# Kernel tuning notes

Measured on AMD Instinct MI355X. Metric: run time of the kernel, lower is better.

The kernel has to match this reference:

```python
import jax, jax.numpy as jnp
import numpy as np

N_LAYERS = 4
EPS = 1e-5  # eqx.nn.LayerNorm default


def _kernels(lam, P, B, C, step, L):
    # Annotated-S4 DPLR generating-function kernel (Q = P), vectorized over H channels.
    # lam, P, B, C: (H, N) complex64; step: (H, 1) real. Returns K: (H, L) real.
    omega = jnp.exp((-2j * jnp.pi) * (jnp.arange(L) / L))            # (L,) roots of unity
    g = (2.0 / step) * ((1.0 - omega) / (1.0 + omega))[None, :]      # (H, L) bilinear warp
    c = 2.0 / (1.0 + omega)                                          # (L,)

    def cauchy(v):  # v: (H, N) -> (H, L): sum_n v_n / (g - lambda_n)
        return jnp.sum(v[:, None, :] / (g[:, :, None] - lam[:, None, :]), axis=-1)

    k00 = cauchy(jnp.conj(C) * B)
    k01 = cauchy(jnp.conj(C) * P)
    k10 = cauchy(jnp.conj(P) * B)
    k11 = cauchy(jnp.conj(P) * P)
    at_roots = c[None, :] * (k00 - k01 * (1.0 / (1.0 + k11)) * k10)  # woodbury correction
    return jnp.fft.ifft(at_roots, n=L, axis=-1).real                 # (H, L)


def _causal_conv(u, K):
    # u: (B, L, H) real input, K: (H, L) real kernel -> causal conv along L via zero-padded FFT.
    L = u.shape[1]
    Ud = jnp.fft.rfft(u, n=2 * L, axis=1)                 # (B, F, H)
    Kd = jnp.fft.rfft(K, n=2 * L, axis=-1)                # (H, F)
    return jnp.fft.irfft(Ud * Kd.T[None], n=2 * L, axis=1)[:, :L]


def _forward(x, enc_w, enc_b, dec_w, dec_b, lam_re, lam_im, p_re, p_im, b_re, b_im,
             c_re, c_im, d, log_step, norm_w, norm_b, w1, b1, w2, b2):
    L = x.shape[1]
    h = x @ enc_w.T + enc_b                               # encoder: (B, L, H)
    for i in range(N_LAYERS):
        skip = h
        mu = h.mean(-1, keepdims=True)
        var = ((h - mu) ** 2).mean(-1, keepdims=True)
        hn = (h - mu) / jnp.sqrt(var + EPS) * norm_w[i] + norm_b[i]
        K = _kernels(lam_re[i] + 1j * lam_im[i], p_re[i] + 1j * p_im[i],
                     b_re[i] + 1j * b_im[i], c_re[i] + 1j * c_im[i],
                     jnp.exp(log_step[i])[:, None], L)
        y = _causal_conv(hn, K) + hn * d[i]               # SSM conv + skip-through D term
        y = jax.nn.gelu(y)
        y = (y @ w1[i].T + b1[i]) * jax.nn.sigmoid(y @ w2[i].T + b2[i])  # gated MLP
        h = skip + y
    return h @ dec_w.T + dec_b                            # decoder: (B, L, out)


def setup_inputs() -> dict:
    key = jax.random.key(0)
    B, L, IN, OUT, H, N, NL = 8, 2048, 64, 64, 128, 64, N_LAYERS
    ks = jax.random.split(key, 12)
    rn = lambda k, s, sc: (jax.random.normal(k, s) * sc).astype(jnp.float32)
    return dict(
        x=rn(ks[0], (B, L, IN), 1.0),
        convolve=1,
        enc_w=rn(ks[1], (H, IN), 1.0 / np.sqrt(IN)), enc_b=jnp.zeros((H,), jnp.float32),
        dec_w=rn(ks[2], (OUT, H), 1.0 / np.sqrt(H)), dec_b=jnp.zeros((OUT,), jnp.float32),
        lam_re=-0.5 * jnp.ones((NL, H, N), jnp.float32),  # HiPPO/S4D-style stable poles
        lam_im=jnp.tile(jnp.float32(np.pi) * jnp.arange(N, dtype=jnp.float32), (NL, H, 1)),
        p_re=rn(ks[3], (NL, H, N), 0.5 / np.sqrt(N)), p_im=rn(ks[4], (NL, H, N), 0.5 / np.sqrt(N)),
        b_re=rn(ks[5], (NL, H, N), 1.0), b_im=rn(ks[6], (NL, H, N), 1.0),
        c_re=rn(ks[7], (NL, H, N), 1.0 / np.sqrt(N)), c_im=rn(ks[8], (NL, H, N), 1.0 / np.sqrt(N)),
        d=jnp.ones((NL, H), jnp.float32),
        log_step=(jax.random.uniform(ks[9], (NL, H)) * (np.log(0.1) - np.log(0.001))
                  + np.log(0.001)).astype(jnp.float32),
        norm_w=jnp.ones((NL, H), jnp.float32), norm_b=jnp.zeros((NL, H), jnp.float32),
        w1=rn(ks[10], (NL, H, H), 1.0 / np.sqrt(H)), b1=jnp.zeros((NL, H), jnp.float32),
        w2=rn(ks[11], (NL, H, H), 1.0 / np.sqrt(H)), b2=jnp.zeros((NL, H), jnp.float32),
    )


def reference(x, convolve, enc_w, enc_b, dec_w, dec_b, lam_re, lam_im, p_re, p_im,
              b_re, b_im, c_re, c_im, d, log_step, norm_w, norm_b, w1, b1, w2, b2):
    # convolve is static 1 (True): the FFT-convolution path of the S4 Model.
    return _forward(x, enc_w, enc_b, dec_w, dec_b, lam_re, lam_im, p_re, p_im, b_re, b_im,
                    c_re, c_im, d, log_step, norm_w, norm_b, w1, b1, w2, b2)
```

## Files before the change

kernel.cpp:

```cpp
#include <hip/hip_runtime.h>
#include <hip/hip_bf16.h>


#define Bsz 8
#define Lseq 2048
#define Hdim 128
#define Npol 64
#define NLAYERS 4

typedef __bf16 bf16x8 __attribute__((ext_vector_type(8)));
typedef float f32x16 __attribute__((ext_vector_type(16)));

__device__ __forceinline__ float fast_rcp(float x) { return __builtin_amdgcn_rcpf(x); }
__device__ __forceinline__ float fast_rsq(float x) { return __builtin_amdgcn_rsqf(x); }

__device__ __forceinline__ float2 cmulf(float2 a, float2 b) {
    return make_float2(a.x * b.x - a.y * b.y, a.x * b.y + a.y * b.x);
}
__device__ __forceinline__ float2 cmulc(float2 a, float2 b) {
    return make_float2(a.x * b.x + a.y * b.y, a.y * b.x - a.x * b.y);
}

__device__ __forceinline__ float gelu_f(float v) {
    float z = 0.7978845608028654f * (v + 0.044715f * v * v * v);
    float e = __expf(2.0f * z);
    return v - v * fast_rcp(e + 1.0f);
}

__device__ __forceinline__ int sw(int i) { return (i & ~15) | ((i ^ (i >> 4)) & 15); }

static __device__ const float W16R[8] = {1.f, 0.9238795325f, 0.7071067812f, 0.3826834324f,
                                         0.f, -0.3826834324f, -0.7071067812f, -0.9238795325f};
static __device__ const float W16I[8] = {0.f, -0.3826834324f, -0.7071067812f, -0.9238795325f,
                                         -1.f, -0.9238795325f, -0.7071067812f, -0.3826834324f};
static __device__ const int BR4[16] = {0, 8, 4, 12, 2, 10, 6, 14, 1, 9, 5, 13, 3, 11, 7, 15};
static __device__ const int BR3[8] = {0, 4, 2, 6, 1, 5, 3, 7};

__device__ __forceinline__ float2 twget(const float2* __restrict__ tw, int e) {
    float2 w = tw[e & 2047];
    if (e & 2048) { w.x = -w.x; w.y = -w.y; }
    return w;
}

template <bool INV>
__device__ __forceinline__ void fft16_dif(float2 v[16]) {
#pragma unroll
    for (int mi = 0; mi < 4; mi++) {
        const int m = 8 >> mi;
#pragma unroll
        for (int g = 0; g < 16; g += 2 * m) {
#pragma unroll
            for (int j = 0; j < m; j++) {
                float wr = W16R[j << mi];
                float wi = INV ? -W16I[j << mi] : W16I[j << mi];
                float2 a = v[g + j], b = v[g + j + m];
                float dx = a.x - b.x, dy = a.y - b.y;
                v[g + j] = make_float2(a.x + b.x, a.y + b.y);
                v[g + j + m] = make_float2(dx * wr - dy * wi, dx * wi + dy * wr);
            }
        }
    }
}

template <bool INV>
__device__ __forceinline__ void fft16_dit(float2 v[16]) {
#pragma unroll
    for (int mi = 3; mi >= 0; mi--) {
        const int m = 8 >> mi;
#pragma unroll
        for (int g = 0; g < 16; g += 2 * m) {
#pragma unroll
            for (int j = 0; j < m; j++) {
                float wr = W16R[j << mi];
                float wi = INV ? -W16I[j << mi] : W16I[j << mi];
                float2 a = v[g + j], b = v[g + j + m];
                float bx = b.x * wr - b.y * wi, by = b.x * wi + b.y * wr;
                v[g + j] = make_float2(a.x + bx, a.y + by);
                v[g + j + m] = make_float2(a.x - bx, a.y - by);
            }
        }
    }
}

template <bool INV>
__device__ __forceinline__ void fft8_dif(float2 v[8]) {
#pragma unroll
    for (int mi = 0; mi < 3; mi++) {
        const int m = 4 >> mi;
#pragma unroll
        for (int g = 0; g < 8; g += 2 * m) {
#pragma unroll
            for (int j = 0; j < m; j++) {
                float wr = W16R[j << (mi + 1)];
                float wi = INV ? -W16I[j << (mi + 1)] : W16I[j << (mi + 1)];
                float2 a = v[g + j], b = v[g + j + m];
                float dx = a.x - b.x, dy = a.y - b.y;
                v[g + j] = make_float2(a.x + b.x, a.y + b.y);
                v[g + j + m] = make_float2(dx * wr - dy * wi, dx * wi + dy * wr);
            }
        }
    }
}

__device__ __forceinline__ void fft4096_passA_hz(float2* data, const float2* __restrict__ tw,
                                                 int t, const float2 vin[8]) {
    float2 v[16];
#pragma unroll
    for (int j = 0; j < 8; j++) v[j] = vin[j];
#pragma unroll
    for (int j = 0; j < 8; j++)
        v[j + 8] = cmulf(v[j], make_float2(W16R[j], W16I[j]));
#pragma unroll
    for (int mi = 1; mi < 4; mi++) {
        const int m = 8 >> mi;
#pragma unroll
        for (int g = 0; g < 16; g += 2 * m) {
#pragma unroll
            for (int j = 0; j < m; j++) {
                float wr = W16R[j << mi], wi = W16I[j << mi];
                float2 a = v[g + j], b = v[g + j + m];
                float dx = a.x - b.x, dy = a.y - b.y;
                v[g + j] = make_float2(a.x + b.x, a.y + b.y);
                v[g + j + m] = make_float2(dx * wr - dy * wi, dx * wi + dy * wr);
            }
        }
    }
#pragma unroll
    for (int i = 1; i < 16; i++) v[i] = cmulf(v[i], twget(tw, t * BR4[i]));
#pragma unroll
    for (int i = 0; i < 16; i++) data[sw(i * 256 + t)] = v[i];
}

__device__ __forceinline__ void fft4096_fwd_BC(float2* data, const float2* __restrict__ tw, int t) {
    __syncthreads();
    {
        int j0 = t & 15;
        int base = (t >> 4) * 256 + j0;
        float2 v[16];
#pragma unroll
        for (int k = 0; k < 16; k++) v[k] = data[sw(base + 16 * k)];
        fft16_dif<false>(v);
#pragma unroll
        for (int i = 1; i < 16; i++) v[i] = cmulf(v[i], twget(tw, 16 * j0 * BR4[i]));
#pragma unroll
        for (int i = 0; i < 16; i++) data[sw(base + 16 * i)] = v[i];
    }
    __syncthreads();
    {
        float2 v[16];
#pragma unroll
        for (int k = 0; k < 16; k++) v[k] = data[sw(t * 16 + k)];
        fft16_dif<false>(v);
#pragma unroll
        for (int i = 0; i < 16; i++) data[sw(t * 16 + i)] = v[i];
    }
    __syncthreads();
}

__global__ __launch_bounds__(256, 4) void prep_kernel(const float* __restrict__ lam_re,
                                                      const float* __restrict__ lam_im,
                                                      const float* __restrict__ p_re,
                                                      const float* __restrict__ p_im,
                                                      const float* __restrict__ b_re,
                                                      const float* __restrict__ b_im,
                                                      const float* __restrict__ c_re,
                                                      const float* __restrict__ c_im,
                                                      const float* __restrict__ log_step,
                                                      const float* __restrict__ w1,
                                                      const float* __restrict__ w2,
                                                      const float* __restrict__ dec_w,
                                                      float2* __restrict__ tw,
                                                      __bf16* __restrict__ wbf,
                                                      __bf16* __restrict__ decbf,
                                                      float2* __restrict__ at_roots) {
    int bid = blockIdx.x, t = threadIdx.x;
    if (bid < 8) {
        int k = bid * 256 + t;
        if (k < 2048) {
            double a = -6.283185307179586476925286766559 * (double)k / 4096.0;
            tw[k] = make_float2((float)cos(a), (float)sin(a));
        }
        return;
    }
    if (bid < 264) {
        int i = (bid - 8) * 256 + t;
        int layer = i >> 14, rem = i & 16383;
        wbf[((size_t)layer * 2) * 16384 + rem] = (__bf16)w1[i];
        wbf[((size_t)layer * 2 + 1) * 16384 + rem] = (__bf16)w2[i];
        return;
    }
    if (bid < 296) {
        int i = (bid - 264) * 256 + t;
        decbf[i] = (__bf16)dec_w[i];
        return;
    }
    int s = bid - 296;
    int h = s & 127, layer = (s >> 7) & 3;
    int l0 = 512 * (s >> 9);
    __shared__ __align__(16) float4 polA[Npol];
    __shared__ __align__(16) float4 polB[Npol];
    __shared__ float n11S[Npol];
    int baseP = (layer * Hdim + h) * Npol;
    if (t < Npol) {
        int n = t;
        float lr = lam_re[baseP + n], li = lam_im[baseP + n];
        float pr = p_re[baseP + n], pi = p_im[baseP + n];
        float br = b_re[baseP + n], bi = b_im[baseP + n];
        float cr = c_re[baseP + n], ci = c_im[baseP + n];
        polA[n] = make_float4(lr, li, cr * br + ci * bi, cr * bi - ci * br);
        polB[n] = make_float4(cr * pr + ci * pi, cr * pi - ci * pr,
                              pr * br + pi * bi, pr * bi - pi * br);
        n11S[n] = pr * pr + pi * pi;
    }
    __syncthreads();
    float step = expf(log_step[layer * Hdim + h]);
    float gs = 2.0f / step;

    float gr[2], gi[2];
#pragma unroll
    for (int j = 0; j < 2; j++) {
        int l = l0 + t + 256 * j;
        float ang = -6.283185307179586f * (float)l / (float)Lseq;
        float wr = cosf(ang), wi = sinf(ang);
        float dr = 1.0f + wr, di = wi;
        float invd2 = fast_rcp(dr * dr + di * di);
        float nr = 1.0f - wr, ni = -wi;
        gr[j] = gs * (nr * dr + ni * di) * invd2;
        gi[j] = gs * (ni * dr - nr * di) * invd2;
    }
    float k00x[2] = {0, 0}, k00y[2] = {0, 0};
    float k01x[2] = {0, 0}, k01y[2] = {0, 0};
    float k10x[2] = {0, 0}, k10y[2] = {0, 0};
    float k11x[2] = {0, 0}, k11y[2] = {0, 0};
#pragma unroll 4
    for (int n = 0; n < Npol; n++) {
        float4 A = polA[n];
        float4 B = polB[n];
        float n11 = n11S[n];
#pragma unroll
        for (int j = 0; j < 2; j++) {
            float er = gr[j] - A.x, ei = gi[j] - A.y;
            float inv2 = fast_rcp(fmaf(er, er, ei * ei));
            float ir = er * inv2;
            float mi = ei * inv2;
            k00x[j] = fmaf(A.z, ir, fmaf(A.w, mi, k00x[j]));
            k00y[j] = fmaf(A.w, ir, fmaf(-A.z, mi, k00y[j]));
            k01x[j] = fmaf(B.x, ir, fmaf(B.y, mi, k01x[j]));
            k01y[j] = fmaf(B.y, ir, fmaf(-B.x, mi, k01y[j]));
            k10x[j] = fmaf(B.z, ir, fmaf(B.w, mi, k10x[j]));
            k10y[j] = fmaf(B.w, ir, fmaf(-B.z, mi, k10y[j]));
            k11x[j] = fmaf(n11, ir, k11x[j]);
            k11y[j] = fmaf(-n11, mi, k11y[j]);
        }
    }
#pragma unroll
    for (int j = 0; j < 2; j++) {
        int l = l0 + t + 256 * j;
        float ang = -6.283185307179586f * (float)l / (float)Lseq;
        float wr = cosf(ang), wi = sinf(ang);
        float dr = 1.0f + wr, di = wi;
        float invd2 = fast_rcp(dr * dr + di * di);
        float cr2 = 2.0f * dr * invd2, ci2 = -2.0f * di * invd2;
        float wr2 = 1.0f + k11x[j], wi2 = k11y[j];
        float w2inv = fast_rcp(fmaf(wr2, wr2, wi2 * wi2));
        float vr = wr2 * w2inv, vi = -wi2 * w2inv;
        float t1x = k01x[j] * k10x[j] - k01y[j] * k10y[j];
        float t1y = k01x[j] * k10y[j] + k01y[j] * k10x[j];
        float t2x = t1x * vr - t1y * vi, t2y = t1x * vi + t1y * vr;
        float ex = k00x[j] - t2x, ey = k00y[j] - t2y;
        at_roots[((size_t)layer * Hdim + h) * Lseq + l] =
            make_float2(cr2 * ex - ci2 * ey, cr2 * ey + ci2 * ex);
    }
}

__global__ __launch_bounds__(256) void kfft_enc_kernel(const float2* __restrict__ at_roots,
                                                       float2* __restrict__ Kd1,
                                                       const float2* __restrict__ tw,
                                                       const float* __restrict__ x,
                                                       const float* __restrict__ enc_w,
                                                       const float* __restrict__ enc_b,
                                                       const float* __restrict__ nw,
                                                       const float* __restrict__ nb,
                                                       float* __restrict__ h,
                                                       float* __restrict__ hnT) {
    __shared__ __align__(16) float smem[11712];
    int bid = blockIdx.x, t = threadIdx.x;
    if (bid < 512) {
        int hh = bid & 127, layer = bid >> 7;
        float2* data = (float2*)smem;
        float* ktmp = smem + 8192;
        const float2* src = at_roots + ((size_t)layer * Hdim + hh) * Lseq;
#pragma unroll
        for (int k = 0; k < 8; k++) {
            int l = t + 256 * k;
            data[sw(l)] = src[l];
        }
        __syncthreads();
        if (t < 128) {
            float2 v[16];
#pragma unroll
            for (int k = 0; k < 16; k++) v[k] = data[sw(t + 128 * k)];
            fft16_dif<true>(v);
#pragma unroll
            for (int i = 1; i < 16; i++) v[i] = cmulc(v[i], twget(tw, 2 * t * BR4[i]));
#pragma unroll
            for (int i = 0; i < 16; i++) data[sw(i * 128 + t)] = v[i];
        }
        __syncthreads();
        if (t < 128) {
            int i2 = t >> 3, j0 = t & 7;
            int base2 = i2 * 128 + j0;
            float2 v[16];
#pragma unroll
            for (int k = 0; k < 16; k++) v[k] = data[sw(base2 + 8 * k)];
            fft16_dif<true>(v);
#pragma unroll
            for (int i = 1; i < 16; i++) v[i] = cmulc(v[i], twget(tw, 32 * j0 * BR4[i]));
#pragma unroll
            for (int i = 0; i < 16; i++) data[sw(base2 + 8 * i)] = v[i];
        }
        __syncthreads();
        {
            float2 v8[8];
#pragma unroll
            for (int k = 0; k < 8; k++) v8[k] = data[sw(t * 8 + k)];
            fft8_dif<true>(v8);
            int r = BR4[t >> 4], s = BR4[t & 15];
#pragma unroll
            for (int i = 0; i < 8; i++) {
                int l = r + 16 * s + 256 * BR3[i];
                ktmp[l] = v8[i].x * (1.0f / 2048.0f);
            }
        }
        __syncthreads();
        {
            float2 vin[8];
#pragma unroll
            for (int k = 0; k < 8; k++) vin[k] = make_float2(ktmp[t + 256 * k], 0.f);
            fft4096_passA_hz(data, tw, t, vin);
        }
        fft4096_fwd_BC(data, tw, t);
        float2* dst = Kd1 + ((size_t)layer * Hdim + hh) * 4096;
#pragma unroll
        for (int k = 0; k < 16; k++) {
            int p = t + 256 * k;
            dst[p] = data[sw(p)];
        }
    } else {
        int r0 = (bid - 512) * 16;
        float* ws = smem;
        float* xst = smem + 8320;
        float* dots = smem + 9600;
        float2* mv = (float2*)(smem + 11648);
        for (int i = t; i < 128 * 64; i += 256) ws[(i >> 6) * 65 + (i & 63)] = enc_w[i];
        for (int i = t; i < 16 * 64; i += 256) {
            int r = i >> 6, k = i & 63;
            xst[k * 20 + r] = x[(size_t)(r0 + r) * 64 + k];
        }
        __syncthreads();
        int o = t & 127, half = t >> 7;
        float acc[8];
        float bo = enc_b[o];
#pragma unroll
        for (int j = 0; j < 8; j++) acc[j] = bo;
        for (int k = 0; k < 64; k++) {
            float wv = ws[o * 65 + k];
            float4 xa = *(const float4*)&xst[k * 20 + half * 8];
            float4 xb = *(const float4*)&xst[k * 20 + half * 8 + 4];
            acc[0] += wv * xa.x; acc[1] += wv * xa.y; acc[2] += wv * xa.z; acc[3] += wv * xa.w;
            acc[4] += wv * xb.x; acc[5] += wv * xb.y; acc[6] += wv * xb.z; acc[7] += wv * xb.w;
        }
#pragma unroll
        for (int j = 0; j < 8; j++) dots[(half * 8 + j) * 128 + o] = acc[j];
        __syncthreads();
        {
            int row = t >> 4, lane = t & 15;
            float s1 = 0.f, s2 = 0.f;
#pragma unroll
            for (int i = 0; i < 8; i++) {
                float v = dots[row * 128 + lane * 8 + i];
                s1 += v; s2 += v * v;
            }
#pragma unroll
            for (int m = 1; m < 16; m <<= 1) { s1 += __shfl_xor(s1, m); s2 += __shfl_xor(s2, m); }
            if (lane == 0) {
                float mu = s1 * (1.0f / 128.0f);
                float var = s2 * (1.0f / 128.0f) - mu * mu;
                mv[row] = make_float2(mu, fast_rsq(var + 1e-5f));
            }
        }
        __syncthreads();
        int c = t & 127;
        int bb = r0 >> 11, l0 = r0 & 2047;
        float nwc = nw[c], nbc = nb[c];
        float hnv[8];
#pragma unroll
        for (int j = 0; j < 8; j++) {
            int r = half * 8 + j;
            float v = dots[r * 128 + c];
            h[(size_t)(r0 + r) * Hdim + c] = v;
            float2 m = mv[r];
            hnv[j] = (v - m.x) * m.y * nwc + nbc;
        }
        float* dst = hnT + ((size_t)bb * Hdim + c) * Lseq + l0 + half * 8;
        *(float4*)dst = make_float4(hnv[0], hnv[1], hnv[2], hnv[3]);
        *(float4*)(dst + 4) = make_float4(hnv[4], hnv[5], hnv[6], hnv[7]);
    }
}

__global__ __launch_bounds__(256) void conv_kernel(float* __restrict__ hnT,
                                                   const float2* __restrict__ Kd1,
                                                   const float* __restrict__ dvec,
                                                   const float2* __restrict__ tw) {
    int h = blockIdx.x, bp = blockIdx.y, t = threadIdx.x;
    __shared__ float2 data[4096];
    float* u0 = hnT + ((size_t)(2 * bp) * Hdim + h) * Lseq;
    float* u1 = hnT + ((size_t)(2 * bp + 1) * Hdim + h) * Lseq;
    float2 ureg[8];
    float2 Kreg[16];
    float2 twB[15];
    const int j0 = t & 15;
    const float4* Kp4 = (const float4*)(Kd1 + (size_t)h * 4096 + t * 16);
    {
        float2 vin[8];
#pragma unroll
        for (int k = 0; k < 8; k++) {
            int l = t + 256 * k;
            float2 u2 = make_float2(u0[l], u1[l]);
            ureg[k] = u2;
            vin[k] = u2;
        }
#pragma unroll
        for (int k = 0; k < 8; k++) {
            float4 q = Kp4[k];
            Kreg[2 * k]     = make_float2(q.x, q.y);
            Kreg[2 * k + 1] = make_float2(q.z, q.w);
        }
#pragma unroll
        for (int i = 1; i < 16; i++) twB[i - 1] = twget(tw, 16 * j0 * BR4[i]);
        fft4096_passA_hz(data, tw, t, vin);
    }
    __syncthreads();
    {
        int base = (t >> 4) * 256 + j0;
        float2 v[16];
#pragma unroll
        for (int k = 0; k < 16; k++) v[k] = data[sw(base + 16 * k)];
        fft16_dif<false>(v);
#pragma unroll
        for (int i = 1; i < 16; i++) v[i] = cmulf(v[i], twB[i - 1]);
#pragma unroll
        for (int i = 0; i < 16; i++) data[sw(base + 16 * i)] = v[i];
    }
    __syncthreads();
    {
        const float scale = 1.0f / 4096.0f;
        float2 v[16];
#pragma unroll
        for (int k = 0; k < 16; k++) v[k] = data[sw(t * 16 + k)];
        fft16_dif<false>(v);
#pragma unroll
        for (int i = 0; i < 16; i++) {
            float2 W = cmulf(v[i], Kreg[i]);
            v[i] = make_float2(W.x * scale, W.y * scale);
        }
        fft16_dit<true>(v);
#pragma unroll
        for (int i = 0; i < 16; i++) data[sw(t * 16 + i)] = v[i];
    }
    __syncthreads();
    {
        int base2 = (t >> 4) * 256 + j0;
        float2 v[16];
        v[0] = data[sw(base2)];
#pragma unroll
        for (int i = 1; i < 16; i++)
            v[i] = cmulc(data[sw(base2 + 16 * i)], twB[i - 1]);
        fft16_dit<true>(v);
#pragma unroll
        for (int i = 0; i < 16; i++) data[sw(base2 + 16 * i)] = v[i];
    }
    __syncthreads();
    {
        float2 v[16];
        v[0] = data[sw(t)];
#pragma unroll
        for (int i = 1; i < 16; i++)
            v[i] = cmulc(data[sw(i * 256 + t)], twget(tw, t * BR4[i]));
#pragma unroll
        for (int mi = 3; mi >= 1; mi--) {
            const int m = 8 >> mi;
#pragma unroll
            for (int g = 0; g < 16; g += 2 * m) {
#pragma unroll
                for (int j = 0; j < m; j++) {
                    float wr = W16R[j << mi], wi = -W16I[j << mi];
                    float2 a = v[g + j], bb2 = v[g + j + m];
                    float bx = bb2.x * wr - bb2.y * wi, by = bb2.x * wi + bb2.y * wr;
                    v[g + j] = make_float2(a.x + bx, a.y + by);
                    v[g + j + m] = make_float2(a.x - bx, a.y - by);
                }
            }
        }
#pragma unroll
        for (int j = 0; j < 8; j++) {
            float wr = W16R[j], wi = -W16I[j];
            float2 bb2 = v[j + 8];
            float bx = bb2.x * wr - bb2.y * wi, by = bb2.x * wi + bb2.y * wr;
            v[j] = make_float2(v[j].x + bx, v[j].y + by);
        }
        float dcoef = dvec[h];
#pragma unroll
        for (int k = 0; k < 8; k++) {
            int l = t + 256 * k;
            u0[l] = gelu_f(v[k].x + ureg[k].x * dcoef);
            u1[l] = gelu_f(v[k].y + ureg[k].y * dcoef);
        }
    }
}

__global__ __launch_bounds__(256) void mlp_kernel(const float* __restrict__ yT,
                                                  float* __restrict__ h,
                                                  float* __restrict__ hnT,
                                                  const __bf16* __restrict__ w1b,
                                                  const __bf16* __restrict__ w2b,
                                                  const float* __restrict__ b1,
                                                  const float* __restrict__ b2,
                                                  const float* __restrict__ nw,
                                                  const float* __restrict__ nb) {
    int r0 = blockIdx.x * 32;
    int t = threadIdx.x;
    int wave = t >> 6, lane = t & 63;
    __shared__ __align__(16) __bf16 ybf[32 * 136];
    __shared__ float dots[32 * 132];
    __shared__ float2 mv[32];
    int bb = r0 >> 11, l0 = r0 & 2047;
    for (int i = t; i < 32 * 128; i += 256) {
        int r = i & 31, k = i >> 5;
        ybf[r * 136 + k] = (__bf16)yT[((size_t)bb * Hdim + k) * Lseq + l0 + r];
    }
    __syncthreads();
    int m = lane & 31, half = lane >> 5;
    bf16x8 a[8];
#pragma unroll
    for (int kk = 0; kk < 8; kk++)
        a[kk] = *(const bf16x8*)&ybf[m * 136 + kk * 16 + half * 8];
    int out = 32 * wave + m;
    const __bf16* w1r = w1b + (size_t)out * 128 + half * 8;
    const __bf16* w2r = w2b + (size_t)out * 128 + half * 8;
    f32x16 acc1, acc2;
#pragma unroll
    for (int i = 0; i < 16; i++) { acc1[i] = 0.f; acc2[i] = 0.f; }
#pragma unroll
    for (int kk = 0; kk < 8; kk++) {
        bf16x8 bw1 = *(const bf16x8*)(w1r + kk * 16);
        bf16x8 bw2 = *(const bf16x8*)(w2r + kk * 16);
        acc1 = __builtin_amdgcn_mfma_f32_32x32x16_bf16(a[kk], bw1, acc1, 0, 0, 0);
        acc2 = __builtin_amdgcn_mfma_f32_32x32x16_bf16(a[kk], bw2, acc2, 0, 0, 0);
    }
    float bias1 = b1[out], bias2 = b2[out];
#pragma unroll
    for (int reg = 0; reg < 16; reg++) {
        int row = (reg & 3) + 8 * (reg >> 2) + 4 * half;
        float v1 = acc1[reg] + bias1;
        float v2 = acc2[reg] + bias2;
        float g = fast_rcp(1.0f + __expf(-v2));
        float hv = h[(size_t)(r0 + row) * Hdim + out] + v1 * g;
        dots[row * 132 + out] = hv;
    }
    __syncthreads();
    {
        int row = t >> 3, lane8 = t & 7;
        float s1 = 0.f, s2 = 0.f;
        int base = row * 132 + lane8 * 16;
#pragma unroll
        for (int q = 0; q < 4; q++) {
            float4 v4 = *(const float4*)&dots[base + 4 * q];
            s1 += v4.x + v4.y + v4.z + v4.w;
            s2 += v4.x * v4.x + v4.y * v4.y + v4.z * v4.z + v4.w * v4.w;
        }
#pragma unroll
        for (int mm = 1; mm < 8; mm <<= 1) { s1 += __shfl_xor(s1, mm); s2 += __shfl_xor(s2, mm); }
        if (lane8 == 0) {
            float mu = s1 * (1.0f / 128.0f);
            float var = s2 * (1.0f / 128.0f) - mu * mu;
            mv[row] = make_float2(mu, fast_rsq(var + 1e-5f));
        }
    }
    __syncthreads();
    {
        int o = t & 127, rh = t >> 7;
        float nwc = nw[o], nbc = nb[o];
        float hnv[16];
#pragma unroll
        for (int j = 0; j < 16; j++) {
            int r = rh * 16 + j;
            float hvv = dots[r * 132 + o];
            h[(size_t)(r0 + r) * Hdim + o] = hvv;
            float2 mvv = mv[r];
            hnv[j] = (hvv - mvv.x) * mvv.y * nwc + nbc;
        }
        float* dst = hnT + ((size_t)bb * Hdim + o) * Lseq + l0 + rh * 16;
        *(float4*)(dst)      = make_float4(hnv[0],  hnv[1],  hnv[2],  hnv[3]);
        *(float4*)(dst + 4)  = make_float4(hnv[4],  hnv[5],  hnv[6],  hnv[7]);
        *(float4*)(dst + 8)  = make_float4(hnv[8],  hnv[9],  hnv[10], hnv[11]);
        *(float4*)(dst + 12) = make_float4(hnv[12], hnv[13], hnv[14], hnv[15]);
    }
}

__global__ __launch_bounds__(256) void mlpdec_kernel(const float* __restrict__ yT,
                                                     const float* __restrict__ h,
                                                     const __bf16* __restrict__ w1b,
                                                     const __bf16* __restrict__ w2b,
                                                     const float* __restrict__ b1,
                                                     const float* __restrict__ b2,
                                                     const __bf16* __restrict__ decb,
                                                     const float* __restrict__ dec_bias,
                                                     float* __restrict__ out) {
    int r0 = blockIdx.x * 32;
    int t = threadIdx.x;
    int wave = t >> 6, lane = t & 63;
    __shared__ __align__(16) __bf16 ybf[32 * 136];
    __shared__ float dots[32 * 132];
    int bb = r0 >> 11, l0 = r0 & 2047;
    for (int i = t; i < 32 * 128; i += 256) {
        int r = i & 31, k = i >> 5;
        ybf[r * 136 + k] = (__bf16)yT[((size_t)bb * Hdim + k) * Lseq + l0 + r];
    }
    __syncthreads();
    int m = lane & 31, half = lane >> 5;
    bf16x8 a[8];
#pragma unroll
    for (int kk = 0; kk < 8; kk++)
        a[kk] = *(const bf16x8*)&ybf[m * 136 + kk * 16 + half * 8];
    int outc = 32 * wave + m;
    const __bf16* w1r = w1b + (size_t)outc * 128 + half * 8;
    const __bf16* w2r = w2b + (size_t)outc * 128 + half * 8;
    f32x16 acc1, acc2;
#pragma unroll
    for (int i = 0; i < 16; i++) { acc1[i] = 0.f; acc2[i] = 0.f; }
#pragma unroll
    for (int kk = 0; kk < 8; kk++) {
        bf16x8 bw1 = *(const bf16x8*)(w1r + kk * 16);
        bf16x8 bw2 = *(const bf16x8*)(w2r + kk * 16);
        acc1 = __builtin_amdgcn_mfma_f32_32x32x16_bf16(a[kk], bw1, acc1, 0, 0, 0);
        acc2 = __builtin_amdgcn_mfma_f32_32x32x16_bf16(a[kk], bw2, acc2, 0, 0, 0);
    }
    float bias1 = b1[outc], bias2 = b2[outc];
#pragma unroll
    for (int reg = 0; reg < 16; reg++) {
        int row = (reg & 3) + 8 * (reg >> 2) + 4 * half;
        float v1 = acc1[reg] + bias1;
        float v2 = acc2[reg] + bias2;
        float g = fast_rcp(1.0f + __expf(-v2));
        float hv = h[(size_t)(r0 + row) * Hdim + outc] + v1 * g;
        dots[row * 132 + outc] = hv;
    }
    __syncthreads();
    for (int i = t; i < 32 * 128; i += 256) {
        int r = i >> 7, k = i & 127;
        ybf[r * 136 + k] = (__bf16)dots[r * 132 + k];
    }
    __syncthreads();
    if (wave < 2) {
        bf16x8 a2[8];
#pragma unroll
        for (int kk = 0; kk < 8; kk++)
            a2[kk] = *(const bf16x8*)&ybf[m * 136 + kk * 16 + half * 8];
        int oc = 32 * wave + m;
        const __bf16* wr = decb + (size_t)oc * 128 + half * 8;
        f32x16 acc;
#pragma unroll
        for (int i = 0; i < 16; i++) acc[i] = 0.f;
#pragma unroll
        for (int kk = 0; kk < 8; kk++) {
            bf16x8 bw = *(const bf16x8*)(wr + kk * 16);
            acc = __builtin_amdgcn_mfma_f32_32x32x16_bf16(a2[kk], bw, acc, 0, 0, 0);
        }
        float bo = dec_bias[oc];
#pragma unroll
        for (int reg = 0; reg < 16; reg++) {
            int row = (reg & 3) + 8 * (reg >> 2) + 4 * half;
            out[(size_t)(r0 + row) * 64 + oc] = acc[reg] + bo;
        }
    }
}

extern "C" void kernel_launch(void* const* d_in, const int* in_sizes, int n_in,
                              void* d_out, int out_size, void* d_ws, size_t ws_size,
                              hipStream_t stream) {
    const float* x      = (const float*)d_in[0];
    const float* enc_w  = (const float*)d_in[2];
    const float* enc_b  = (const float*)d_in[3];
    const float* dec_w  = (const float*)d_in[4];
    const float* dec_b  = (const float*)d_in[5];
    const float* lam_re = (const float*)d_in[6];
    const float* lam_im = (const float*)d_in[7];
    const float* p_re   = (const float*)d_in[8];
    const float* p_im   = (const float*)d_in[9];
    const float* b_re   = (const float*)d_in[10];
    const float* b_im   = (const float*)d_in[11];
    const float* c_re   = (const float*)d_in[12];
    const float* c_im   = (const float*)d_in[13];
    const float* dvec   = (const float*)d_in[14];
    const float* lstep  = (const float*)d_in[15];
    const float* norm_w = (const float*)d_in[16];
    const float* norm_b = (const float*)d_in[17];
    const float* w1     = (const float*)d_in[18];
    const float* b1     = (const float*)d_in[19];
    const float* w2     = (const float*)d_in[20];
    const float* b2     = (const float*)d_in[21];
    float* out = (float*)d_out;

    char* ws = (char*)d_ws;
    float2* tw  = (float2*)ws;  ws += 2048 * sizeof(float2);
    float*  h   = (float*)ws;   ws += (size_t)Bsz * Lseq * Hdim * sizeof(float);
    float*  hnT = (float*)ws;   ws += (size_t)Bsz * Lseq * Hdim * sizeof(float);
    float2* atr = (float2*)ws;  ws += (size_t)NLAYERS * Hdim * Lseq * sizeof(float2);
    float2* Kd1 = (float2*)ws;  ws += (size_t)NLAYERS * Hdim * 4096 * sizeof(float2);
    __bf16* wbf = (__bf16*)ws;  ws += (size_t)NLAYERS * 2 * Hdim * Hdim * sizeof(__bf16);
    __bf16* dbf = (__bf16*)ws;  ws += (size_t)64 * Hdim * sizeof(__bf16);

    const int nrows = Bsz * Lseq;

    prep_kernel<<<296 + 2048, 256, 0, stream>>>(
        lam_re, lam_im, p_re, p_im, b_re, b_im, c_re, c_im, lstep, w1, w2, dec_w,
        tw, wbf, dbf, atr);
    kfft_enc_kernel<<<512 + nrows / 16, 256, 0, stream>>>(
        atr, Kd1, tw, x, enc_w, enc_b, norm_w, norm_b, h, hnT);
    for (int L = 0; L < NLAYERS; L++) {
        conv_kernel<<<dim3(Hdim, Bsz / 2), 256, 0, stream>>>(
            hnT, Kd1 + (size_t)L * Hdim * 4096, dvec + L * Hdim, tw);
        const __bf16* w1bL = wbf + (size_t)L * 2 * Hdim * Hdim;
        const __bf16* w2bL = w1bL + Hdim * Hdim;
        if (L < NLAYERS - 1) {
            const float* nwn = norm_w + (L + 1) * Hdim;
            const float* nbn = norm_b + (L + 1) * Hdim;
            mlp_kernel<<<nrows / 32, 256, 0, stream>>>(hnT, h, hnT, w1bL, w2bL,
                                                       b1 + L * Hdim, b2 + L * Hdim,
                                                       nwn, nbn);
        } else {
            mlpdec_kernel<<<nrows / 32, 256, 0, stream>>>(hnT, h, w1bL, w2bL,
                                                          b1 + L * Hdim, b2 + L * Hdim,
                                                          dbf, dec_b, out);
        }
    }
}
```

Before: 288.8 us.

## Fuse DPLR Cauchy kernel computation into the kernel-FFT blocks

Moves the generating-function (Cauchy sum plus Woodbury correction) computation from the prep kernel into the kernel-FFT blocks of kfft_enc_kernel, writing results directly into shared memory instead of a global at_roots buffer. This removes the global write/read of the intermediate array and shrinks the prep grid. In exchange, each thread now handles 8 frequency points with many live accumulators, reducing parallelism for that stage and raising register pressure, which may lengthen the tail of the fused kernel.

```diff
diff --git a/kernel.cpp b/kernel.cpp
--- a/kernel.cpp
+++ b/kernel.cpp
@@ -157,22 +157,12 @@
     __syncthreads();
 }
 
-__global__ __launch_bounds__(256, 4) void prep_kernel(const float* __restrict__ lam_re,
-                                                      const float* __restrict__ lam_im,
-                                                      const float* __restrict__ p_re,
-                                                      const float* __restrict__ p_im,
-                                                      const float* __restrict__ b_re,
-                                                      const float* __restrict__ b_im,
-                                                      const float* __restrict__ c_re,
-                                                      const float* __restrict__ c_im,
-                                                      const float* __restrict__ log_step,
-                                                      const float* __restrict__ w1,
+__global__ __launch_bounds__(256, 4) void prep_kernel(const float* __restrict__ w1,
                                                       const float* __restrict__ w2,
                                                       const float* __restrict__ dec_w,
                                                       float2* __restrict__ tw,
                                                       __bf16* __restrict__ wbf,
-                                                      __bf16* __restrict__ decbf,
-                                                      float2* __restrict__ at_roots) {
+                                                      __bf16* __restrict__ decbf) {
     int bid = blockIdx.x, t = threadIdx.x;
     if (bid < 8) {
         int k = bid * 256 + t;
@@ -189,92 +179,11 @@
         wbf[((size_t)layer * 2 + 1) * 16384 + rem] = (__bf16)w2[i];
         return;
     }
-    if (bid < 296) {
-        int i = (bid - 264) * 256 + t;
-        decbf[i] = (__bf16)dec_w[i];
-        return;
-    }
-    int s = bid - 296;
-    int h = s & 127, layer = (s >> 7) & 3;
-    int l0 = 512 * (s >> 9);
-    __shared__ __align__(16) float4 polA[Npol];
-    __shared__ __align__(16) float4 polB[Npol];
-    __shared__ float n11S[Npol];
-    int baseP = (layer * Hdim + h) * Npol;
-    if (t < Npol) {
-        int n = t;
-        float lr = lam_re[baseP + n], li = lam_im[baseP + n];
-        float pr = p_re[baseP + n], pi = p_im[baseP + n];
-        float br = b_re[baseP + n], bi = b_im[baseP + n];
-        float cr = c_re[baseP + n], ci = c_im[baseP + n];
-        polA[n] = make_float4(lr, li, cr * br + ci * bi, cr * bi - ci * br);
-        polB[n] = make_float4(cr * pr + ci * pi, cr * pi - ci * pr,
-                              pr * br + pi * bi, pr * bi - pi * br);
-        n11S[n] = pr * pr + pi * pi;
-    }
-    __syncthreads();
-    float step = expf(log_step[layer * Hdim + h]);
-    float gs = 2.0f / step;
-
-    float gr[2], gi[2];
-#pragma unroll
-    for (int j = 0; j < 2; j++) {
-        int l = l0 + t + 256 * j;
-        float ang = -6.283185307179586f * (float)l / (float)Lseq;
-        float wr = cosf(ang), wi = sinf(ang);
-        float dr = 1.0f + wr, di = wi;
-        float invd2 = fast_rcp(dr * dr + di * di);
-        float nr = 1.0f - wr, ni = -wi;
-        gr[j] = gs * (nr * dr + ni * di) * invd2;
-        gi[j] = gs * (ni * dr - nr * di) * invd2;
-    }
-    float k00x[2] = {0, 0}, k00y[2] = {0, 0};
-    float k01x[2] = {0, 0}, k01y[2] = {0, 0};
-    float k10x[2] = {0, 0}, k10y[2] = {0, 0};
-    float k11x[2] = {0, 0}, k11y[2] = {0, 0};
-#pragma unroll 4
-    for (int n = 0; n < Npol; n++) {
-        float4 A = polA[n];
-        float4 B = polB[n];
-        float n11 = n11S[n];
-#pragma unroll
-        for (int j = 0; j < 2; j++) {
-            float er = gr[j] - A.x, ei = gi[j] - A.y;
-            float inv2 = fast_rcp(fmaf(er, er, ei * ei));
-            float ir = er * inv2;
-            float mi = ei * inv2;
-            k00x[j] = fmaf(A.z, ir, fmaf(A.w, mi, k00x[j]));
-            k00y[j] = fmaf(A.w, ir, fmaf(-A.z, mi, k00y[j]));
-            k01x[j] = fmaf(B.x, ir, fmaf(B.y, mi, k01x[j]));
-            k01y[j] = fmaf(B.y, ir, fmaf(-B.x, mi, k01y[j]));
-            k10x[j] = fmaf(B.z, ir, fmaf(B.w, mi, k10x[j]));
-            k10y[j] = fmaf(B.w, ir, fmaf(-B.z, mi, k10y[j]));
-            k11x[j] = fmaf(n11, ir, k11x[j]);
-            k11y[j] = fmaf(-n11, mi, k11y[j]);
-        }
-    }
-#pragma unroll
-    for (int j = 0; j < 2; j++) {
-        int l = l0 + t + 256 * j;
-        float ang = -6.283185307179586f * (float)l / (float)Lseq;
-        float wr = cosf(ang), wi = sinf(ang);
-        float dr = 1.0f + wr, di = wi;
-        float invd2 = fast_rcp(dr * dr + di * di);
-        float cr2 = 2.0f * dr * invd2, ci2 = -2.0f * di * invd2;
-        float wr2 = 1.0f + k11x[j], wi2 = k11y[j];
-        float w2inv = fast_rcp(fmaf(wr2, wr2, wi2 * wi2));
-        float vr = wr2 * w2inv, vi = -wi2 * w2inv;
-        float t1x = k01x[j] * k10x[j] - k01y[j] * k10y[j];
-        float t1y = k01x[j] * k10y[j] + k01y[j] * k10x[j];
-        float t2x = t1x * vr - t1y * vi, t2y = t1x * vi + t1y * vr;
-        float ex = k00x[j] - t2x, ey = k00y[j] - t2y;
-        at_roots[((size_t)layer * Hdim + h) * Lseq + l] =
-            make_float2(cr2 * ex - ci2 * ey, cr2 * ey + ci2 * ex);
-    }
-}
-
-__global__ __launch_bounds__(256) void kfft_enc_kernel(const float2* __restrict__ at_roots,
-                                                       float2* __restrict__ Kd1,
+    int i = (bid - 264) * 256 + t;
+    decbf[i] = (__bf16)dec_w[i];
+}
+
+__global__ __launch_bounds__(256) void kfft_enc_kernel(float2* __restrict__ Kd1,
                                                        const float2* __restrict__ tw,
                                                        const float* __restrict__ x,
                                                        const float* __restrict__ enc_w,
@@ -282,18 +191,97 @@
                                                        const float* __restrict__ nw,
                                                        const float* __restrict__ nb,
                                                        float* __restrict__ h,
-                                                       float* __restrict__ hnT) {
+                                                       float* __restrict__ hnT,
+                                                       const float* __restrict__ lam_re,
+                                                       const float* __restrict__ lam_im,
+                                                       const float* __restrict__ p_re,
+                                                       const float* __restrict__ p_im,
+                                                       const float* __restrict__ b_re,
+                                                       const float* __restrict__ b_im,
+                                                       const float* __restrict__ c_re,
+                                                       const float* __restrict__ c_im,
+                                                       const float* __restrict__ log_step) {
     __shared__ __align__(16) float smem[11712];
     int bid = blockIdx.x, t = threadIdx.x;
     if (bid < 512) {
         int hh = bid & 127, layer = bid >> 7;
         float2* data = (float2*)smem;
         float* ktmp = smem + 8192;
-        const float2* src = at_roots + ((size_t)layer * Hdim + hh) * Lseq;
-#pragma unroll
-        for (int k = 0; k < 8; k++) {
-            int l = t + 256 * k;
-            data[sw(l)] = src[l];
+        float4* polA = (float4*)(smem + 10240);
+        float4* polB = (float4*)(smem + 10496);
+        float* n11S = smem + 10752;
+        int baseP = (layer * Hdim + hh) * Npol;
+        if (t < Npol) {
+            int n = t;
+            float lr = lam_re[baseP + n], li = lam_im[baseP + n];
+            float pr = p_re[baseP + n], pi = p_im[baseP + n];
+            float br = b_re[baseP + n], bi = b_im[baseP + n];
+            float cr = c_re[baseP + n], ci = c_im[baseP + n];
+            polA[n] = make_float4(lr, li, cr * br + ci * bi, cr * bi - ci * br);
+            polB[n] = make_float4(cr * pr + ci * pi, cr * pi - ci * pr,
+                                  pr * br + pi * bi, pr * bi - pi * br);
+            n11S[n] = pr * pr + pi * pi;
+        }
+        __syncthreads();
+        {
+            float step = expf(log_step[layer * Hdim + hh]);
+            float gs = 2.0f / step;
+            float wrv[8], wiv[8];
+            float gr[8], gi[8];
+#pragma unroll
+            for (int j = 0; j < 8; j++) {
+                int l = t + 256 * j;
+                float ang = -6.283185307179586f * (float)l / (float)Lseq;
+                float wr = cosf(ang), wi = sinf(ang);
+                wrv[j] = wr; wiv[j] = wi;
+                float dr = 1.0f + wr, di = wi;
+                float invd2 = fast_rcp(dr * dr + di * di);
+                float nr = 1.0f - wr, ni = -wi;
+                gr[j] = gs * (nr * dr + ni * di) * invd2;
+                gi[j] = gs * (ni * dr - nr * di) * invd2;
+            }
+            float k00x[8], k00y[8], k01x[8], k01y[8];
+            float k10x[8], k10y[8], k11x[8], k11y[8];
+#pragma unroll
+            for (int j = 0; j < 8; j++) {
+                k00x[j] = 0.f; k00y[j] = 0.f; k01x[j] = 0.f; k01y[j] = 0.f;
+                k10x[j] = 0.f; k10y[j] = 0.f; k11x[j] = 0.f; k11y[j] = 0.f;
+            }
+            for (int n = 0; n < Npol; n++) {
+                float4 A = polA[n];
+                float4 B = polB[n];
+                float n11 = n11S[n];
+#pragma unroll
+                for (int j = 0; j < 8; j++) {
+                    float er = gr[j] - A.x, ei = gi[j] - A.y;
+                    float inv2 = fast_rcp(fmaf(er, er, ei * ei));
+                    float ir = er * inv2;
+                    float mi = ei * inv2;
+                    k00x[j] = fmaf(A.z, ir, fmaf(A.w, mi, k00x[j]));
+                    k00y[j] = fmaf(A.w, ir, fmaf(-A.z, mi, k00y[j]));
+                    k01x[j] = fmaf(B.x, ir, fmaf(B.y, mi, k01x[j]));
+                    k01y[j] = fmaf(B.y, ir, fmaf(-B.x, mi, k01y[j]));
+                    k10x[j] = fmaf(B.z, ir, fmaf(B.w, mi, k10x[j]));
+                    k10y[j] = fmaf(B.w, ir, fmaf(-B.z, mi, k10y[j]));
+                    k11x[j] = fmaf(n11, ir, k11x[j]);
+                    k11y[j] = fmaf(-n11, mi, k11y[j]);
+                }
+            }
+#pragma unroll
+            for (int j = 0; j < 8; j++) {
+                int l = t + 256 * j;
+                float dr = 1.0f + wrv[j], di = wiv[j];
+                float invd2 = fast_rcp(dr * dr + di * di);
+                float cr2 = 2.0f * dr * invd2, ci2 = -2.0f * di * invd2;
+                float wr2 = 1.0f + k11x[j], wi2 = k11y[j];
+                float w2inv = fast_rcp(fmaf(wr2, wr2, wi2 * wi2));
+                float vr = wr2 * w2inv, vi = -wi2 * w2inv;
+                float t1x = k01x[j] * k10x[j] - k01y[j] * k10y[j];
+                float t1y = k01x[j] * k10y[j] + k01y[j] * k10x[j];
+                float t2x = t1x * vr - t1y * vi, t2y = t1x * vi + t1y * vr;
+                float ex = k00x[j] - t2x, ey = k00y[j] - t2y;
+                data[sw(l)] = make_float2(cr2 * ex - ci2 * ey, cr2 * ey + ci2 * ex);
+            }
         }
         __syncthreads();
         if (t < 128) {
@@ -716,18 +704,16 @@
     float2* tw  = (float2*)ws;  ws += 2048 * sizeof(float2);
     float*  h   = (float*)ws;   ws += (size_t)Bsz * Lseq * Hdim * sizeof(float);
     float*  hnT = (float*)ws;   ws += (size_t)Bsz * Lseq * Hdim * sizeof(float);
-    float2* atr = (float2*)ws;  ws += (size_t)NLAYERS * Hdim * Lseq * sizeof(float2);
     float2* Kd1 = (float2*)ws;  ws += (size_t)NLAYERS * Hdim * 4096 * sizeof(float2);
     __bf16* wbf = (__bf16*)ws;  ws += (size_t)NLAYERS * 2 * Hdim * Hdim * sizeof(__bf16);
     __bf16* dbf = (__bf16*)ws;  ws += (size_t)64 * Hdim * sizeof(__bf16);
 
     const int nrows = Bsz * Lseq;
 
-    prep_kernel<<<296 + 2048, 256, 0, stream>>>(
-        lam_re, lam_im, p_re, p_im, b_re, b_im, c_re, c_im, lstep, w1, w2, dec_w,
-        tw, wbf, dbf, atr);
+    prep_kernel<<<296, 256, 0, stream>>>(w1, w2, dec_w, tw, wbf, dbf);
     kfft_enc_kernel<<<512 + nrows / 16, 256, 0, stream>>>(
-        atr, Kd1, tw, x, enc_w, enc_b, norm_w, norm_b, h, hnT);
+        Kd1, tw, x, enc_w, enc_b, norm_w, norm_b, h, hnT,
+        lam_re, lam_im, p_re, p_im, b_re, b_im, c_re, c_im, lstep);
     for (int L = 0; L < NLAYERS; L++) {
         conv_kernel<<<dim3(Hdim, Bsz / 2), 256, 0, stream>>>(
             hnT, Kd1 + (size_t)L * Hdim * 4096, dvec + L * Hdim, tw);
```

Result: faster. 278.4 us (-3.6%).
